# Optimization experiments

Measured on AMD Instinct MI355X. Metric: run time of the kernel, lower is better.

Reference implementation:

```python
import jax, jax.numpy as jnp
import numpy as np

N = 100000      # nodes
E = 1250000     # edges
DIN = 128       # input_feature_dim
H = 64          # hidden_feature_dim
C = 16          # num_classes
BN_EPS = 1e-5


def _linear_init(key, fin, fout):
    # torch.nn.Linear default: U(-1/sqrt(fin), 1/sqrt(fin)); stored as [fin, fout] for x @ W
    s = 1.0 / np.sqrt(fin)
    kw, kb = jax.random.split(key)
    w = jax.random.uniform(kw, (fin, fout), jnp.float32, -s, s)
    b = jax.random.uniform(kb, (fout,), jnp.float32, -s, s)
    return w, b


def setup_inputs() -> dict:
    key = jax.random.key(0)
    ks = jax.random.split(key, 16)
    inp = {}
    inp["x"] = jax.random.normal(ks[0], (N, DIN), jnp.float32)
    src = jax.random.randint(ks[1], (E,), 0, N)
    dst = jax.random.randint(ks[2], (E,), 0, N)
    inp["edge_index"] = jnp.stack([src, dst]).astype(jnp.int64)
    inp["fc1_w"], inp["fc1_b"] = _linear_init(ks[3], DIN, H)
    dims = [(H, H), (H, H), (H, C)]
    for i, (fi, fo) in enumerate(dims):
        w, b = _linear_init(ks[4 + i], fi, fo)
        inp[f"conv{i}_w"] = w
        inp[f"conv{i}_b"] = b
        inp[f"bn{i}_g"] = jnp.ones((fo,), jnp.float32)
        inp[f"bn{i}_b"] = jnp.zeros((fo,), jnp.float32)
    inp["fc2_w"], inp["fc2_b"] = _linear_init(ks[7], C, C)
    return inp


def gcn_conv(h, w, b, src, dst, n):
    # PyG GCNConv: linear transform, add self-loops, symmetric normalization,
    # scatter-add messages from src into dst, then add bias.
    h = h @ w                                   # [N, out]
    loops = jnp.arange(n)
    s = jnp.concatenate([src, loops])           # [E+N]
    d = jnp.concatenate([dst, loops])
    deg = jax.ops.segment_sum(jnp.ones(s.shape[0], h.dtype), d, num_segments=n)
    dinv = jnp.where(deg > 0, jax.lax.rsqrt(deg), 0.0)
    norm = dinv[s] * dinv[d]                    # [E+N]
    msg = h[s] * norm[:, None]                  # [E+N, out] gather + scale
    out = jax.ops.segment_sum(msg, d, num_segments=n)
    return out + b


def batch_norm(x, gamma, beta):
    # BatchNorm1d in training mode: biased batch statistics over nodes
    mu = x.mean(axis=0)
    var = x.var(axis=0)
    return (x - mu) * jax.lax.rsqrt(var + BN_EPS) * gamma + beta


def reference(x, edge_index, fc1_w, fc1_b,
              conv0_w, conv0_b, bn0_g, bn0_b,
              conv1_w, conv1_b, bn1_g, bn1_b,
              conv2_w, conv2_b, bn2_g, bn2_b,
              fc2_w, fc2_b):
    src, dst = edge_index[0], edge_index[1]
    n = x.shape[0]
    h = jax.nn.relu(x @ fc1_w + fc1_b)
    layers = [(conv0_w, conv0_b, bn0_g, bn0_b),
              (conv1_w, conv1_b, bn1_g, bn1_b),
              (conv2_w, conv2_b, bn2_g, bn2_b)]
    for w, b, g, be in layers:
        h = jax.nn.relu(batch_norm(gcn_conv(h, w, b, src, dst, n), g, be))
    h = h @ fc2_w + fc2_b
    return jax.nn.log_softmax(h, axis=1)
```

## Files before the change

kernel.cpp:

```cpp
#include <hip/hip_runtime.h>

#define BN_EPS 1e-5f

typedef unsigned int uint32;

__device__ __forceinline__ void fma4(float4& a, float s, const float4& w) {
    a.x = fmaf(s, w.x, a.x); a.y = fmaf(s, w.y, a.y);
    a.z = fmaf(s, w.z, a.z); a.w = fmaf(s, w.w, a.w);
}

__device__ __forceinline__ float blo(uint32 p) { return __uint_as_float(p << 16); }
__device__ __forceinline__ float bhi(uint32 p) { return __uint_as_float(p & 0xFFFF0000u); }
__device__ __forceinline__ uint32 f2bf1(float f) {
    uint32 u = __float_as_uint(f);
    return (u + 0x7FFFu + ((u >> 16) & 1u)) >> 16;
}
__device__ __forceinline__ uint32 packbf(float a, float b) { return f2bf1(a) | (f2bf1(b) << 16); }


__global__ __launch_bounds__(256) void k_deg_count(const int* __restrict__ dst, int* deg, int e) {
    int i = blockIdx.x * 256 + threadIdx.x;
    if (i < e) atomicAdd(&deg[dst[i]], 1);
}


__global__ __launch_bounds__(256) void k_scan1(const int* __restrict__ deg, int* __restrict__ off,
                                               int* __restrict__ bsum, float* __restrict__ dinv, int n) {
    __shared__ int sh[256];
    int i = blockIdx.x * 256 + threadIdx.x;
    int v = (i < n) ? deg[i] : 0;
    if (i < n) dinv[i] = rsqrtf((float)v + 1.0f);
    sh[threadIdx.x] = v;
    __syncthreads();
    #pragma unroll
    for (int d = 1; d < 256; d <<= 1) {
        int t = (threadIdx.x >= d) ? sh[threadIdx.x - d] : 0;
        __syncthreads();
        sh[threadIdx.x] += t;
        __syncthreads();
    }
    if (i < n) off[i] = sh[threadIdx.x] - v;
    if (threadIdx.x == 255) bsum[blockIdx.x] = sh[255];
}

__global__ __launch_bounds__(512) void k_scan2(int* bsum, int nb) {
    __shared__ int sh[512];
    int v = (threadIdx.x < nb) ? bsum[threadIdx.x] : 0;
    sh[threadIdx.x] = v;
    __syncthreads();
    #pragma unroll
    for (int d = 1; d < 512; d <<= 1) {
        int t = (threadIdx.x >= d) ? sh[threadIdx.x - d] : 0;
        __syncthreads();
        sh[threadIdx.x] += t;
        __syncthreads();
    }
    if (threadIdx.x < nb) bsum[threadIdx.x] = sh[threadIdx.x] - v;
}

__global__ __launch_bounds__(256) void k_scan3(int* __restrict__ off, const int* __restrict__ bsum,
                                               int* __restrict__ cnt, int n, int e) {
    int i = blockIdx.x * 256 + threadIdx.x;
    if (i < n) { off[i] += bsum[blockIdx.x]; cnt[i] = 0; }
    if (i == 0) off[n] = e;
}

__global__ __launch_bounds__(256) void k_fill(const int* __restrict__ src, const int* __restrict__ dst,
                                              const int* __restrict__ off, int* __restrict__ cnt,
                                              int* __restrict__ esrc, int e) {
    int i = blockIdx.x * 256 + threadIdx.x;
    if (i < e) {
        int d = dst[i];
        int slot = off[d] + atomicAdd(&cnt[d], 1);
        esrc[slot] = src[i];
    }
}


template<int FIN, int FOUT, bool RELU, bool BIAS, bool BNIN, bool DSCALE, bool OBF>
__global__ __launch_bounds__(256) void k_linear(const float* __restrict__ X, const float* __restrict__ W,
                                                const float* __restrict__ bias, void* __restrict__ Yv,
                                                const float* __restrict__ S, const float* __restrict__ bng,
                                                const float* __restrict__ bnb, const float* __restrict__ dinv,
                                                float inv_n, int n) {
    constexpr int KC = 64;
    constexpr int TX = FOUT / 4;
    constexpr int TY = 256 / TX;
    constexpr int RQ = (FOUT == 64) ? 4 : 2;
    constexpr int TILE_R = TY * RQ;
    constexpr int LDX = KC + 4;
    constexpr int LDW = FOUT + 4;
    __shared__ float Xs[TILE_R][LDX];
    __shared__ float Ws[KC][LDW];
    __shared__ float scs[BNIN ? FIN : 4], sfs[BNIN ? FIN : 4];

    const int tx = threadIdx.x % TX;
    const int ty = threadIdx.x / TX;

    if (BNIN) {
        for (int c = threadIdx.x; c < FIN; c += 256) {
            float mu = S[c] * inv_n;
            float var = S[FIN + c] * inv_n - mu * mu;
            float is = rsqrtf(var + BN_EPS) * bng[c];
            scs[c] = is;
            sfs[c] = bnb[c] - mu * is;
        }
        __syncthreads();
    }

    float4 bb = make_float4(0.f, 0.f, 0.f, 0.f);
    if (BIAS) bb = *(const float4*)(bias + tx * 4);

    for (int r0 = blockIdx.x * TILE_R; r0 < n; r0 += gridDim.x * TILE_R) {
        float4 acc[RQ];
        #pragma unroll
        for (int q = 0; q < RQ; ++q) acc[q] = bb;

        for (int kc = 0; kc < FIN; kc += KC) {
            __syncthreads();
            for (int idx = threadIdx.x; idx < TILE_R * (KC / 4); idx += 256) {
                int rr = idx / (KC / 4), k4 = idx % (KC / 4);
                int row = r0 + rr;
                float4 v = make_float4(0.f, 0.f, 0.f, 0.f);
                if (row < n) v = *(const float4*)(X + (size_t)row * FIN + kc + 4 * k4);
                if (BNIN) {
                    int c = kc + 4 * k4;
                    v.x = fmaxf(fmaf(v.x, scs[c+0], sfs[c+0]), 0.f);
                    v.y = fmaxf(fmaf(v.y, scs[c+1], sfs[c+1]), 0.f);
                    v.z = fmaxf(fmaf(v.z, scs[c+2], sfs[c+2]), 0.f);
                    v.w = fmaxf(fmaf(v.w, scs[c+3], sfs[c+3]), 0.f);
                }
                *(float4*)(&Xs[rr][4 * k4]) = v;
            }
            for (int idx = threadIdx.x; idx < KC * (FOUT / 4); idx += 256) {
                int kk = idx / (FOUT / 4), c4 = idx % (FOUT / 4);
                *(float4*)(&Ws[kk][4 * c4]) = *(const float4*)(W + (size_t)(kc + kk) * FOUT + 4 * c4);
            }
            __syncthreads();

            #pragma unroll 4
            for (int k4 = 0; k4 < KC / 4; ++k4) {
                float4 w0 = *(const float4*)(&Ws[4*k4+0][tx*4]);
                float4 w1 = *(const float4*)(&Ws[4*k4+1][tx*4]);
                float4 w2 = *(const float4*)(&Ws[4*k4+2][tx*4]);
                float4 w3 = *(const float4*)(&Ws[4*k4+3][tx*4]);
                #pragma unroll
                for (int q = 0; q < RQ; ++q) {
                    float4 xv = *(const float4*)(&Xs[ty*RQ+q][4*k4]);
                    fma4(acc[q], xv.x, w0);
                    fma4(acc[q], xv.y, w1);
                    fma4(acc[q], xv.z, w2);
                    fma4(acc[q], xv.w, w3);
                }
            }
        }

        #pragma unroll
        for (int q = 0; q < RQ; ++q) {
            int row = r0 + ty * RQ + q;
            if (row < n) {
                float4 v = acc[q];
                if (RELU) {
                    v.x = fmaxf(v.x, 0.f); v.y = fmaxf(v.y, 0.f);
                    v.z = fmaxf(v.z, 0.f); v.w = fmaxf(v.w, 0.f);
                }
                if (DSCALE) {
                    float dv = dinv[row];
                    v.x *= dv; v.y *= dv; v.z *= dv; v.w *= dv;
                }
                if (OBF) {
                    uint2 pk;
                    pk.x = packbf(v.x, v.y);
                    pk.y = packbf(v.z, v.w);
                    ((uint2*)Yv)[(size_t)row * (FOUT / 4) + tx] = pk;
                } else {
                    *(float4*)((float*)Yv + (size_t)row * FOUT + tx * 4) = v;
                }
            }
        }
    }
}


__global__ __launch_bounds__(256) void k_accum64bf(const uint2* __restrict__ Tb2, const int* __restrict__ esrc,
                                                   const int* __restrict__ off, const float* __restrict__ dinv,
                                                   const float* __restrict__ bias, float* __restrict__ Z,
                                                   float* __restrict__ S, int n) {
    const int lane = threadIdx.x & 63;
    const int wid  = threadIdx.x >> 6;
    const int lp   = lane & 15;
    const int es   = lane >> 4;
    const float4 bb = *(const float4*)(bias + 4 * lp);
    float st1[4] = {0.f,0.f,0.f,0.f}, st2[4] = {0.f,0.f,0.f,0.f};
    const uint2 z2 = make_uint2(0u, 0u);

    for (int dp = blockIdx.x * 4 + wid; 2 * dp < n; dp += gridDim.x * 4) {
        const int dA = 2 * dp, dB = 2 * dp + 1;
        const int oA0 = off[dA], oA1 = off[dA + 1];
        const int oB0 = oA1;
        const int oB1 = (dB < n) ? off[dB + 1] : oA1;

        float aA0=0.f, aA1=0.f, aA2=0.f, aA3=0.f;
        float aB0=0.f, aB1=0.f, aB2=0.f, aB3=0.f;
        int bA = oA0, bB = oB0;
        while (bA < oA1 || bB < oB1) {
            if (bA < oA1) {
                int i0 = bA + 4 * es;
                int s0 = (i0     < oA1) ? esrc[i0]     : -1;
                int s1 = (i0 + 1 < oA1) ? esrc[i0 + 1] : -1;
                int s2 = (i0 + 2 < oA1) ? esrc[i0 + 2] : -1;
                int s3 = (i0 + 3 < oA1) ? esrc[i0 + 3] : -1;
                uint2 p0 = (s0 >= 0) ? Tb2[(size_t)s0 * 16 + lp] : z2;
                uint2 p1 = (s1 >= 0) ? Tb2[(size_t)s1 * 16 + lp] : z2;
                uint2 p2 = (s2 >= 0) ? Tb2[(size_t)s2 * 16 + lp] : z2;
                uint2 p3 = (s3 >= 0) ? Tb2[(size_t)s3 * 16 + lp] : z2;
                aA0 += (blo(p0.x) + blo(p1.x)) + (blo(p2.x) + blo(p3.x));
                aA1 += (bhi(p0.x) + bhi(p1.x)) + (bhi(p2.x) + bhi(p3.x));
                aA2 += (blo(p0.y) + blo(p1.y)) + (blo(p2.y) + blo(p3.y));
                aA3 += (bhi(p0.y) + bhi(p1.y)) + (bhi(p2.y) + bhi(p3.y));
            }
            if (bB < oB1) {
                int i0 = bB + 4 * es;
                int s0 = (i0     < oB1) ? esrc[i0]     : -1;
                int s1 = (i0 + 1 < oB1) ? esrc[i0 + 1] : -1;
                int s2 = (i0 + 2 < oB1) ? esrc[i0 + 2] : -1;
                int s3 = (i0 + 3 < oB1) ? esrc[i0 + 3] : -1;
                uint2 p0 = (s0 >= 0) ? Tb2[(size_t)s0 * 16 + lp] : z2;
                uint2 p1 = (s1 >= 0) ? Tb2[(size_t)s1 * 16 + lp] : z2;
                uint2 p2 = (s2 >= 0) ? Tb2[(size_t)s2 * 16 + lp] : z2;
                uint2 p3 = (s3 >= 0) ? Tb2[(size_t)s3 * 16 + lp] : z2;
                aB0 += (blo(p0.x) + blo(p1.x)) + (blo(p2.x) + blo(p3.x));
                aB1 += (bhi(p0.x) + bhi(p1.x)) + (bhi(p2.x) + bhi(p3.x));
                aB2 += (blo(p0.y) + blo(p1.y)) + (blo(p2.y) + blo(p3.y));
                aB3 += (bhi(p0.y) + bhi(p1.y)) + (bhi(p2.y) + bhi(p3.y));
            }
            bA += 16; bB += 16;
        }

        aA0 += __shfl_xor(aA0, 16); aA0 += __shfl_xor(aA0, 32);
        aA1 += __shfl_xor(aA1, 16); aA1 += __shfl_xor(aA1, 32);
        aA2 += __shfl_xor(aA2, 16); aA2 += __shfl_xor(aA2, 32);
        aA3 += __shfl_xor(aA3, 16); aA3 += __shfl_xor(aA3, 32);
        aB0 += __shfl_xor(aB0, 16); aB0 += __shfl_xor(aB0, 32);
        aB1 += __shfl_xor(aB1, 16); aB1 += __shfl_xor(aB1, 32);
        aB2 += __shfl_xor(aB2, 16); aB2 += __shfl_xor(aB2, 32);
        aB3 += __shfl_xor(aB3, 16); aB3 += __shfl_xor(aB3, 32);

        if (es == 0) {
            uint2 ps = Tb2[(size_t)dA * 16 + lp];
            float dv = dinv[dA];
            float4 zz;
            zz.x = fmaf(aA0 + blo(ps.x), dv, bb.x);
            zz.y = fmaf(aA1 + bhi(ps.x), dv, bb.y);
            zz.z = fmaf(aA2 + blo(ps.y), dv, bb.z);
            zz.w = fmaf(aA3 + bhi(ps.y), dv, bb.w);
            *(float4*)(Z + (size_t)dA * 64 + 4 * lp) = zz;
            st1[0] += zz.x; st2[0] += zz.x * zz.x;
            st1[1] += zz.y; st2[1] += zz.y * zz.y;
            st1[2] += zz.z; st2[2] += zz.z * zz.z;
            st1[3] += zz.w; st2[3] += zz.w * zz.w;
            if (dB < n) {
                uint2 pb = Tb2[(size_t)dB * 16 + lp];
                float dvB = dinv[dB];
                float4 zb;
                zb.x = fmaf(aB0 + blo(pb.x), dvB, bb.x);
                zb.y = fmaf(aB1 + bhi(pb.x), dvB, bb.y);
                zb.z = fmaf(aB2 + blo(pb.y), dvB, bb.z);
                zb.w = fmaf(aB3 + bhi(pb.y), dvB, bb.w);
                *(float4*)(Z + (size_t)dB * 64 + 4 * lp) = zb;
                st1[0] += zb.x; st2[0] += zb.x * zb.x;
                st1[1] += zb.y; st2[1] += zb.y * zb.y;
                st1[2] += zb.z; st2[2] += zb.z * zb.z;
                st1[3] += zb.w; st2[3] += zb.w * zb.w;
            }
        }
    }

    __shared__ float sh1[4][64], sh2[4][64];
    if (es == 0) {
        *(float4*)(&sh1[wid][4 * lp]) = make_float4(st1[0], st1[1], st1[2], st1[3]);
        *(float4*)(&sh2[wid][4 * lp]) = make_float4(st2[0], st2[1], st2[2], st2[3]);
    }
    __syncthreads();
    if (threadIdx.x < 64) {
        float t1 = 0.f, t2 = 0.f;
        #pragma unroll
        for (int w = 0; w < 4; ++w) { t1 += sh1[w][threadIdx.x]; t2 += sh2[w][threadIdx.x]; }
        atomicAdd(&S[threadIdx.x], t1);
        atomicAdd(&S[64 + threadIdx.x], t2);
    }
}


__global__ __launch_bounds__(256) void k_accum16bf(const uint2* __restrict__ Tb2, const int* __restrict__ esrc,
                                                   const int* __restrict__ off, const float* __restrict__ dinv,
                                                   const float* __restrict__ bias, float* __restrict__ Z,
                                                   float* __restrict__ S, int n) {
    const int lane = threadIdx.x & 63;
    const int wid  = threadIdx.x >> 6;
    const int lp   = lane & 3;
    const int es   = lane >> 2;
    const float4 bb = *(const float4*)(bias + 4 * lp);
    float st1[4] = {0.f,0.f,0.f,0.f}, st2[4] = {0.f,0.f,0.f,0.f};
    const uint2 z2 = make_uint2(0u, 0u);

    for (int dp = blockIdx.x * 4 + wid; 2 * dp < n; dp += gridDim.x * 4) {
        const int dA = 2 * dp, dB = 2 * dp + 1;
        const int oA0 = off[dA], oA1 = off[dA + 1];
        const int oB0 = oA1;
        const int oB1 = (dB < n) ? off[dB + 1] : oA1;

        float aA0=0.f, aA1=0.f, aA2=0.f, aA3=0.f;
        float aB0=0.f, aB1=0.f, aB2=0.f, aB3=0.f;
        int bA = oA0, bB = oB0;
        while (bA < oA1 || bB < oB1) {
            if (bA < oA1) {
                int i0 = bA + es;
                int s0 = (i0 < oA1) ? esrc[i0] : -1;
                uint2 p0 = (s0 >= 0) ? Tb2[(size_t)s0 * 4 + lp] : z2;
                aA0 += blo(p0.x); aA1 += bhi(p0.x); aA2 += blo(p0.y); aA3 += bhi(p0.y);
            }
            if (bB < oB1) {
                int i0 = bB + es;
                int s0 = (i0 < oB1) ? esrc[i0] : -1;
                uint2 p0 = (s0 >= 0) ? Tb2[(size_t)s0 * 4 + lp] : z2;
                aB0 += blo(p0.x); aB1 += bhi(p0.x); aB2 += blo(p0.y); aB3 += bhi(p0.y);
            }
            bA += 16; bB += 16;
        }

        #pragma unroll
        for (int sh = 4; sh <= 32; sh <<= 1) {
            aA0 += __shfl_xor(aA0, sh); aA1 += __shfl_xor(aA1, sh);
            aA2 += __shfl_xor(aA2, sh); aA3 += __shfl_xor(aA3, sh);
            aB0 += __shfl_xor(aB0, sh); aB1 += __shfl_xor(aB1, sh);
            aB2 += __shfl_xor(aB2, sh); aB3 += __shfl_xor(aB3, sh);
        }

        if (es == 0) {
            uint2 ps = Tb2[(size_t)dA * 4 + lp];
            float dv = dinv[dA];
            float4 zz;
            zz.x = fmaf(aA0 + blo(ps.x), dv, bb.x);
            zz.y = fmaf(aA1 + bhi(ps.x), dv, bb.y);
            zz.z = fmaf(aA2 + blo(ps.y), dv, bb.z);
            zz.w = fmaf(aA3 + bhi(ps.y), dv, bb.w);
            *(float4*)(Z + (size_t)dA * 16 + 4 * lp) = zz;
            st1[0] += zz.x; st2[0] += zz.x * zz.x;
            st1[1] += zz.y; st2[1] += zz.y * zz.y;
            st1[2] += zz.z; st2[2] += zz.z * zz.z;
            st1[3] += zz.w; st2[3] += zz.w * zz.w;
            if (dB < n) {
                uint2 pb = Tb2[(size_t)dB * 4 + lp];
                float dvB = dinv[dB];
                float4 zb;
                zb.x = fmaf(aB0 + blo(pb.x), dvB, bb.x);
                zb.y = fmaf(aB1 + bhi(pb.x), dvB, bb.y);
                zb.z = fmaf(aB2 + blo(pb.y), dvB, bb.z);
                zb.w = fmaf(aB3 + bhi(pb.y), dvB, bb.w);
                *(float4*)(Z + (size_t)dB * 16 + 4 * lp) = zb;
                st1[0] += zb.x; st2[0] += zb.x * zb.x;
                st1[1] += zb.y; st2[1] += zb.y * zb.y;
                st1[2] += zb.z; st2[2] += zb.z * zb.z;
                st1[3] += zb.w; st2[3] += zb.w * zb.w;
            }
        }
    }

    __shared__ float sh1[4][16], sh2[4][16];
    if (es == 0) {
        *(float4*)(&sh1[wid][4 * lp]) = make_float4(st1[0], st1[1], st1[2], st1[3]);
        *(float4*)(&sh2[wid][4 * lp]) = make_float4(st2[0], st2[1], st2[2], st2[3]);
    }
    __syncthreads();
    if (threadIdx.x < 16) {
        float t1 = 0.f, t2 = 0.f;
        #pragma unroll
        for (int w = 0; w < 4; ++w) { t1 += sh1[w][threadIdx.x]; t2 += sh2[w][threadIdx.x]; }
        atomicAdd(&S[threadIdx.x], t1);
        atomicAdd(&S[16 + threadIdx.x], t2);
    }
}


__global__ __launch_bounds__(256) void k_fc2_lsm(const float* __restrict__ Hin, const float* __restrict__ W,
                                                 const float* __restrict__ bias, const float* __restrict__ S,
                                                 const float* __restrict__ bng, const float* __restrict__ bnb,
                                                 float inv_n, float* __restrict__ out, int n) {
    __shared__ float Ws[256];
    __shared__ float bs[16], sc[16], sf[16];
    Ws[threadIdx.x] = W[threadIdx.x];
    if (threadIdx.x < 16) {
        int c = threadIdx.x;
        bs[c] = bias[c];
        float mu = S[c] * inv_n;
        float var = S[16 + c] * inv_n - mu * mu;
        float is = rsqrtf(var + BN_EPS) * bng[c];
        sc[c] = is;
        sf[c] = bnb[c] - mu * is;
    }
    __syncthreads();
    for (int row = blockIdx.x * 256 + threadIdx.x; row < n; row += gridDim.x * 256) {
        float h[16];
        const float4* hp = (const float4*)(Hin + (size_t)row * 16);
        #pragma unroll
        for (int q = 0; q < 4; ++q) {
            float4 h4 = hp[q];
            h[q*4+0] = h4.x; h[q*4+1] = h4.y; h[q*4+2] = h4.z; h[q*4+3] = h4.w;
        }
        #pragma unroll
        for (int k = 0; k < 16; ++k) h[k] = fmaxf(fmaf(h[k], sc[k], sf[k]), 0.0f);
        float o[16];
        #pragma unroll
        for (int c = 0; c < 16; ++c) {
            float acc = bs[c];
            #pragma unroll
            for (int k = 0; k < 16; ++k) acc += h[k] * Ws[k * 16 + c];
            o[c] = acc;
        }
        float m = o[0];
        #pragma unroll
        for (int c = 1; c < 16; ++c) m = fmaxf(m, o[c]);
        float ssum = 0.f;
        #pragma unroll
        for (int c = 0; c < 16; ++c) ssum += expf(o[c] - m);
        float lse = m + logf(ssum);
        float4* op = (float4*)(out + (size_t)row * 16);
        #pragma unroll
        for (int q = 0; q < 4; ++q) {
            float4 w4;
            w4.x = o[q*4+0] - lse; w4.y = o[q*4+1] - lse;
            w4.z = o[q*4+2] - lse; w4.w = o[q*4+3] - lse;
            op[q] = w4;
        }
    }
}


extern "C" void kernel_launch(void* const* d_in, const int* in_sizes, int n_in,
                              void* d_out, int out_size, void* d_ws, size_t ws_size,
                              hipStream_t stream) {
    const float* x      = (const float*)d_in[0];
    const int*   ei     = (const int*)d_in[1];
    const float* fc1_w  = (const float*)d_in[2];
    const float* fc1_b  = (const float*)d_in[3];
    const float* conv_w[3] = { (const float*)d_in[4],  (const float*)d_in[8],  (const float*)d_in[12] };
    const float* conv_b[3] = { (const float*)d_in[5],  (const float*)d_in[9],  (const float*)d_in[13] };
    const float* bn_g[3]   = { (const float*)d_in[6],  (const float*)d_in[10], (const float*)d_in[14] };
    const float* bn_b[3]   = { (const float*)d_in[7],  (const float*)d_in[11], (const float*)d_in[15] };
    const float* fc2_w  = (const float*)d_in[16];
    const float* fc2_b  = (const float*)d_in[17];

    const int n = in_sizes[0] / 128;
    const int e = in_sizes[1] / 2;
    const int* src = ei;
    const int* dst = ei + e;
    const float inv_n = 1.0f / (float)n;

    float*  A    = (float*)d_ws;
    float*  Bf   = A + (size_t)n * 64;
    uint2*  Bb2  = (uint2*)Bf;
    float*  dinv = Bf + (size_t)n * 64;
    int*    deg  = (int*)(dinv + n);
    int*    off  = deg + n;
    int*    esrc = off + n + 1;
    float*  stats = (float*)(esrc + e);
    int*    bsum = (int*)(stats + 384);

    const int gN  = (n + 255) / 256;
    const int gE  = (e + 255) / 256;
    const int gAcc = 2048;
    const int gLin64 = (n + 63) / 64;
    const int gLin128 = (n + 127) / 128;

    float* st[3] = { stats, stats + 128, stats + 256 };

    hipMemsetAsync(deg, 0, (size_t)n * sizeof(int), stream);
    hipMemsetAsync(stats, 0, 384 * sizeof(float), stream);
    k_deg_count<<<gE, 256, 0, stream>>>(dst, deg, e);
    k_scan1<<<gN, 256, 0, stream>>>(deg, off, bsum, dinv, n);
    k_scan2<<<1, 512, 0, stream>>>(bsum, gN);
    k_scan3<<<gN, 256, 0, stream>>>(off, bsum, deg , n, e);
    k_fill<<<gE, 256, 0, stream>>>(src, dst, off, deg , esrc, e);

    k_linear<128, 64, true, true, false, false, false><<<gLin64, 256, 0, stream>>>(
        x, fc1_w, fc1_b, A, nullptr, nullptr, nullptr, nullptr, 0.f, n);

    k_linear<64, 64, false, false, false, true, true><<<gLin64, 256, 0, stream>>>(
        A, conv_w[0], nullptr, Bb2, nullptr, nullptr, nullptr, dinv, 0.f, n);
    k_accum64bf<<<gAcc, 256, 0, stream>>>(Bb2, esrc, off, dinv, conv_b[0], A, st[0], n);

    k_linear<64, 64, false, false, true, true, true><<<gLin64, 256, 0, stream>>>(
        A, conv_w[1], nullptr, Bb2, st[0], bn_g[0], bn_b[0], dinv, inv_n, n);
    k_accum64bf<<<gAcc, 256, 0, stream>>>(Bb2, esrc, off, dinv, conv_b[1], A, st[1], n);

    k_linear<64, 16, false, false, true, true, true><<<gLin128, 256, 0, stream>>>(
        A, conv_w[2], nullptr, Bb2, st[1], bn_g[1], bn_b[1], dinv, inv_n, n);
    k_accum16bf<<<gAcc, 256, 0, stream>>>(Bb2, esrc, off, dinv, conv_b[2], A, st[2], n);

    k_fc2_lsm<<<gLin64, 256, 0, stream>>>(A, fc2_w, fc2_b, st[2], bn_g[2], bn_b[2], inv_n, (float*)d_out, n);
}
```

Before: 498.0 us.

## Rewrite 64-wide aggregation as merge-path style contiguous edge ranges per wave

The 64-feature CSR aggregation kernel now gives each wave a contiguous range of destination nodes and streams that range's edges in 8-edge tiles. Each tile is a full 128-byte bf16 row per edge, loaded as uint4 and triple-buffered in registers. Tiles are staged through a per-wave LDS ring, and then each lane accumulates one feature column serially, flushing a node's output whenever the edge cursor crosses its CSR boundary. The aim is to replace the two-node-per-wave, degree-padded gather with fully coalesced row loads and to balance edges more evenly. The cost is a serial per-edge inner loop with branches on node boundaries, and there are no explicit wave syncs around the shared ring.

```diff
diff --git a/kernel.cpp b/kernel.cpp
--- a/kernel.cpp
+++ b/kernel.cpp
@@ -182,110 +182,101 @@
 }
 
 
-__global__ __launch_bounds__(256) void k_accum64bf(const uint2* __restrict__ Tb2, const int* __restrict__ esrc,
+__global__ __launch_bounds__(256) void k_accum64bf(const uint32* __restrict__ Tb, const int* __restrict__ esrc,
                                                    const int* __restrict__ off, const float* __restrict__ dinv,
                                                    const float* __restrict__ bias, float* __restrict__ Z,
-                                                   float* __restrict__ S, int n) {
+                                                   float* __restrict__ S, int n, int npw) {
+    __shared__ uint32 ring[4][2][256];
+    __shared__ float sA[4][64], sB[4][64];
+
     const int lane = threadIdx.x & 63;
     const int wid  = threadIdx.x >> 6;
-    const int lp   = lane & 15;
-    const int es   = lane >> 4;
-    const float4 bb = *(const float4*)(bias + 4 * lp);
-    float st1[4] = {0.f,0.f,0.f,0.f}, st2[4] = {0.f,0.f,0.f,0.f};
-    const uint2 z2 = make_uint2(0u, 0u);
-
-    for (int dp = blockIdx.x * 4 + wid; 2 * dp < n; dp += gridDim.x * 4) {
-        const int dA = 2 * dp, dB = 2 * dp + 1;
-        const int oA0 = off[dA], oA1 = off[dA + 1];
-        const int oB0 = oA1;
-        const int oB1 = (dB < n) ? off[dB + 1] : oA1;
-
-        float aA0=0.f, aA1=0.f, aA2=0.f, aA3=0.f;
-        float aB0=0.f, aB1=0.f, aB2=0.f, aB3=0.f;
-        int bA = oA0, bB = oB0;
-        while (bA < oA1 || bB < oB1) {
-            if (bA < oA1) {
-                int i0 = bA + 4 * es;
-                int s0 = (i0     < oA1) ? esrc[i0]     : -1;
-                int s1 = (i0 + 1 < oA1) ? esrc[i0 + 1] : -1;
-                int s2 = (i0 + 2 < oA1) ? esrc[i0 + 2] : -1;
-                int s3 = (i0 + 3 < oA1) ? esrc[i0 + 3] : -1;
-                uint2 p0 = (s0 >= 0) ? Tb2[(size_t)s0 * 16 + lp] : z2;
-                uint2 p1 = (s1 >= 0) ? Tb2[(size_t)s1 * 16 + lp] : z2;
-                uint2 p2 = (s2 >= 0) ? Tb2[(size_t)s2 * 16 + lp] : z2;
-                uint2 p3 = (s3 >= 0) ? Tb2[(size_t)s3 * 16 + lp] : z2;
-                aA0 += (blo(p0.x) + blo(p1.x)) + (blo(p2.x) + blo(p3.x));
-                aA1 += (bhi(p0.x) + bhi(p1.x)) + (bhi(p2.x) + bhi(p3.x));
-                aA2 += (blo(p0.y) + blo(p1.y)) + (blo(p2.y) + blo(p3.y));
-                aA3 += (bhi(p0.y) + bhi(p1.y)) + (bhi(p2.y) + bhi(p3.y));
-            }
-            if (bB < oB1) {
-                int i0 = bB + 4 * es;
-                int s0 = (i0     < oB1) ? esrc[i0]     : -1;
-                int s1 = (i0 + 1 < oB1) ? esrc[i0 + 1] : -1;
-                int s2 = (i0 + 2 < oB1) ? esrc[i0 + 2] : -1;
-                int s3 = (i0 + 3 < oB1) ? esrc[i0 + 3] : -1;
-                uint2 p0 = (s0 >= 0) ? Tb2[(size_t)s0 * 16 + lp] : z2;
-                uint2 p1 = (s1 >= 0) ? Tb2[(size_t)s1 * 16 + lp] : z2;
-                uint2 p2 = (s2 >= 0) ? Tb2[(size_t)s2 * 16 + lp] : z2;
-                uint2 p3 = (s3 >= 0) ? Tb2[(size_t)s3 * 16 + lp] : z2;
-                aB0 += (blo(p0.x) + blo(p1.x)) + (blo(p2.x) + blo(p3.x));
-                aB1 += (bhi(p0.x) + bhi(p1.x)) + (bhi(p2.x) + bhi(p3.x));
-                aB2 += (blo(p0.y) + blo(p1.y)) + (blo(p2.y) + blo(p3.y));
-                aB3 += (bhi(p0.y) + bhi(p1.y)) + (bhi(p2.y) + bhi(p3.y));
-            }
-            bA += 16; bB += 16;
-        }
-
-        aA0 += __shfl_xor(aA0, 16); aA0 += __shfl_xor(aA0, 32);
-        aA1 += __shfl_xor(aA1, 16); aA1 += __shfl_xor(aA1, 32);
-        aA2 += __shfl_xor(aA2, 16); aA2 += __shfl_xor(aA2, 32);
-        aA3 += __shfl_xor(aA3, 16); aA3 += __shfl_xor(aA3, 32);
-        aB0 += __shfl_xor(aB0, 16); aB0 += __shfl_xor(aB0, 32);
-        aB1 += __shfl_xor(aB1, 16); aB1 += __shfl_xor(aB1, 32);
-        aB2 += __shfl_xor(aB2, 16); aB2 += __shfl_xor(aB2, 32);
-        aB3 += __shfl_xor(aB3, 16); aB3 += __shfl_xor(aB3, 32);
-
-        if (es == 0) {
-            uint2 ps = Tb2[(size_t)dA * 16 + lp];
-            float dv = dinv[dA];
-            float4 zz;
-            zz.x = fmaf(aA0 + blo(ps.x), dv, bb.x);
-            zz.y = fmaf(aA1 + bhi(ps.x), dv, bb.y);
-            zz.z = fmaf(aA2 + blo(ps.y), dv, bb.z);
-            zz.w = fmaf(aA3 + bhi(ps.y), dv, bb.w);
-            *(float4*)(Z + (size_t)dA * 64 + 4 * lp) = zz;
-            st1[0] += zz.x; st2[0] += zz.x * zz.x;
-            st1[1] += zz.y; st2[1] += zz.y * zz.y;
-            st1[2] += zz.z; st2[2] += zz.z * zz.z;
-            st1[3] += zz.w; st2[3] += zz.w * zz.w;
-            if (dB < n) {
-                uint2 pb = Tb2[(size_t)dB * 16 + lp];
-                float dvB = dinv[dB];
-                float4 zb;
-                zb.x = fmaf(aB0 + blo(pb.x), dvB, bb.x);
-                zb.y = fmaf(aB1 + bhi(pb.x), dvB, bb.y);
-                zb.z = fmaf(aB2 + blo(pb.y), dvB, bb.z);
-                zb.w = fmaf(aB3 + bhi(pb.y), dvB, bb.w);
-                *(float4*)(Z + (size_t)dB * 64 + 4 * lp) = zb;
-                st1[0] += zb.x; st2[0] += zb.x * zb.x;
-                st1[1] += zb.y; st2[1] += zb.y * zb.y;
-                st1[2] += zb.z; st2[2] += zb.z * zb.z;
-                st1[3] += zb.w; st2[3] += zb.w * zb.w;
-            }
-        }
-    }
-
-    __shared__ float sh1[4][64], sh2[4][64];
-    if (es == 0) {
-        *(float4*)(&sh1[wid][4 * lp]) = make_float4(st1[0], st1[1], st1[2], st1[3]);
-        *(float4*)(&sh2[wid][4 * lp]) = make_float4(st2[0], st2[1], st2[2], st2[3]);
-    }
+    const int rsub = lane >> 3;
+    const int csub = lane & 7;
+    const int cidx = lane >> 1;
+    const int chal = lane & 1;
+    const float bcol = bias[lane];
+
+    float s1 = 0.f, s2 = 0.f;
+
+    const int gw = blockIdx.x * 4 + wid;
+    const int d0 = gw * npw;
+
+    if (d0 < n) {
+        const int d1 = min(d0 + npw, n);
+        const int e0 = off[d0];
+        const int e1 = off[d1];
+        const int nt = (e1 - e0 + 7) >> 3;
+
+        uint32* slot0 = &ring[wid][0][0];
+        uint32* slot1 = &ring[wid][1][0];
+
+        int d = d0;
+        int nxt = off[d + 1];
+        uint32 selfp = Tb[(size_t)d * 32 + cidx];
+        float  dv    = dinv[d];
+        float  part  = 0.f;
+        int    ec    = e0;
+
+        auto tload = [&](int t) -> uint4 {
+            int ei = min(e0 + t * 8 + rsub, e1 - 1);
+            int s = esrc[ei];
+            return ((const uint4*)Tb)[(size_t)s * 8 + csub];
+        };
+
+        uint4 B0, B1, B2;
+        if (nt > 0) B0 = tload(0);
+        if (nt > 1) B1 = tload(1);
+        if (nt > 2) B2 = tload(2);
+
+        for (int t = 0; t < nt; ++t) {
+            uint32* sl = (t & 1) ? slot1 : slot0;
+            uint4 cur = (t % 3 == 0) ? B0 : (t % 3 == 1) ? B1 : B2;
+            *(uint4*)(sl + lane * 4) = cur;
+            if (t + 3 < nt) {
+                if (t % 3 == 0) B0 = tload(t + 3);
+                else if (t % 3 == 1) B1 = tload(t + 3);
+                else B2 = tload(t + 3);
+            }
+            int rend = min(8, e1 - (e0 + t * 8));
+            for (int r = 0; r < rend; ++r) {
+                while (ec == nxt) {
+                    float sv = chal ? bhi(selfp) : blo(selfp);
+                    float z = fmaf(part + sv, dv, bcol);
+                    Z[(size_t)d * 64 + lane] = z;
+                    s1 += z; s2 += z * z;
+                    part = 0.f;
+                    ++d;
+                    nxt = off[d + 1];
+                    selfp = Tb[(size_t)d * 32 + cidx];
+                    dv = dinv[d];
+                }
+                uint32 p = sl[r * 32 + cidx];
+                part += chal ? bhi(p) : blo(p);
+                ++ec;
+            }
+        }
+        while (d < d1) {
+            float sv = chal ? bhi(selfp) : blo(selfp);
+            float z = fmaf(part + sv, dv, bcol);
+            Z[(size_t)d * 64 + lane] = z;
+            s1 += z; s2 += z * z;
+            part = 0.f;
+            ++d;
+            if (d < d1) {
+                selfp = Tb[(size_t)d * 32 + cidx];
+                dv = dinv[d];
+            }
+        }
+    }
+
+    sA[wid][lane] = s1;
+    sB[wid][lane] = s2;
     __syncthreads();
     if (threadIdx.x < 64) {
         float t1 = 0.f, t2 = 0.f;
         #pragma unroll
-        for (int w = 0; w < 4; ++w) { t1 += sh1[w][threadIdx.x]; t2 += sh2[w][threadIdx.x]; }
+        for (int w = 0; w < 4; ++w) { t1 += sA[w][threadIdx.x]; t2 += sB[w][threadIdx.x]; }
         atomicAdd(&S[threadIdx.x], t1);
         atomicAdd(&S[64 + threadIdx.x], t2);
     }
@@ -459,6 +450,7 @@
 
     float*  A    = (float*)d_ws;
     float*  Bf   = A + (size_t)n * 64;
+    uint32* Bb   = (uint32*)Bf;
     uint2*  Bb2  = (uint2*)Bf;
     float*  dinv = Bf + (size_t)n * 64;
     int*    deg  = (int*)(dinv + n);
@@ -470,6 +462,8 @@
     const int gN  = (n + 255) / 256;
     const int gE  = (e + 255) / 256;
     const int gAcc = 2048;
+    const int nwaves = gAcc * 4;
+    const int npw = (n + nwaves - 1) / nwaves;
     const int gLin64 = (n + 63) / 64;
     const int gLin128 = (n + 127) / 128;
 
@@ -487,12 +481,12 @@
         x, fc1_w, fc1_b, A, nullptr, nullptr, nullptr, nullptr, 0.f, n);
 
     k_linear<64, 64, false, false, false, true, true><<<gLin64, 256, 0, stream>>>(
-        A, conv_w[0], nullptr, Bb2, nullptr, nullptr, nullptr, dinv, 0.f, n);
-    k_accum64bf<<<gAcc, 256, 0, stream>>>(Bb2, esrc, off, dinv, conv_b[0], A, st[0], n);
+        A, conv_w[0], nullptr, Bb, nullptr, nullptr, nullptr, dinv, 0.f, n);
+    k_accum64bf<<<gAcc, 256, 0, stream>>>(Bb, esrc, off, dinv, conv_b[0], A, st[0], n, npw);
 
     k_linear<64, 64, false, false, true, true, true><<<gLin64, 256, 0, stream>>>(
-        A, conv_w[1], nullptr, Bb2, st[0], bn_g[0], bn_b[0], dinv, inv_n, n);
-    k_accum64bf<<<gAcc, 256, 0, stream>>>(Bb2, esrc, off, dinv, conv_b[1], A, st[1], n);
+        A, conv_w[1], nullptr, Bb, st[0], bn_g[0], bn_b[0], dinv, inv_n, n);
+    k_accum64bf<<<gAcc, 256, 0, stream>>>(Bb, esrc, off, dinv, conv_b[1], A, st[1], n, npw);
 
     k_linear<64, 16, false, false, true, true, true><<<gLin128, 256, 0, stream>>>(
         A, conv_w[2], nullptr, Bb2, st[1], bn_g[1], bn_b[1], dinv, inv_n, n);
```

After: 502.2 us. No clear change (+0.8%).
